# Kernel optimization log

Measured on AMD Instinct MI355X. Metric: run time of the kernel, lower is better.

The kernel has to match this reference:

```python
import jax, jax.numpy as jnp
import numpy as np

D, DFF, H, NLAYERS, B, L, U = 1536, 2048, 8, 2, 16, 64, 64
EPS = 1e-5


def _ln(x, w, b):
    mu = jnp.mean(x, axis=-1, keepdims=True)
    var = jnp.mean((x - mu) ** 2, axis=-1, keepdims=True)
    return (x - mu) / jnp.sqrt(var + EPS) * w + b


def _mha(q_in, kv_in, qkv_w, qkv_b, out_w, out_b, mask):
    # torch nn.MultiheadAttention: packed in_proj [3D,D], out_proj [D,D]
    d = q_in.shape[-1]
    hd = d // H
    wq, wk, wv = jnp.split(qkv_w, 3, axis=0)
    bq, bk, bv = jnp.split(qkv_b, 3, axis=0)
    q = q_in @ wq.T + bq
    k = kv_in @ wk.T + bk
    v = kv_in @ wv.T + bv
    def heads(t):
        b_, s_, _ = t.shape
        return t.reshape(b_, s_, H, hd).transpose(0, 2, 1, 3)  # [B,H,S,hd]
    q, k, v = heads(q), heads(k), heads(v)
    scores = jnp.einsum('bhqd,bhkd->bhqk', q, k) / jnp.sqrt(jnp.float32(hd))
    if mask is not None:
        scores = scores + mask  # [Sq,Sk] broadcast
    attn = jax.nn.softmax(scores, axis=-1)
    o = jnp.einsum('bhqk,bhkd->bhqd', attn, v)
    b_, _, s_, _ = o.shape
    o = o.transpose(0, 2, 1, 3).reshape(b_, s_, d)
    return o @ out_w.T + out_b


def setup_inputs() -> dict:
    key = jax.random.key(0)
    ks = jax.random.split(key, 16)
    f = lambda k, shp: (jax.random.normal(k, shp, jnp.float32) * 0.02)
    Lyr = NLAYERS
    return {
        'x': jax.random.normal(ks[0], (B, L, U, D), jnp.float32),
        'pooler_w': f(ks[1], (1, D)),
        'pooler_b': jnp.zeros((1,), jnp.float32),
        'pos_embed': f(ks[2], (1, 128, D)),
        'sa_qkv_w': f(ks[3], (Lyr, 3 * D, D)),
        'sa_qkv_b': jnp.zeros((Lyr, 3 * D), jnp.float32),
        'sa_out_w': f(ks[4], (Lyr, D, D)),
        'sa_out_b': jnp.zeros((Lyr, D), jnp.float32),
        'ca_qkv_w': f(ks[5], (Lyr, 3 * D, D)),
        'ca_qkv_b': jnp.zeros((Lyr, 3 * D), jnp.float32),
        'ca_out_w': f(ks[6], (Lyr, D, D)),
        'ca_out_b': jnp.zeros((Lyr, D), jnp.float32),
        'ff1_w': f(ks[7], (Lyr, DFF, D)),
        'ff1_b': jnp.zeros((Lyr, DFF), jnp.float32),
        'ff2_w': f(ks[8], (Lyr, D, DFF)),
        'ff2_b': jnp.zeros((Lyr, D), jnp.float32),
        'ln1_w': jnp.ones((Lyr, D), jnp.float32),
        'ln1_b': jnp.zeros((Lyr, D), jnp.float32),
        'ln2_w': jnp.ones((Lyr, D), jnp.float32),
        'ln2_b': jnp.zeros((Lyr, D), jnp.float32),
        'ln3_w': jnp.ones((Lyr, D), jnp.float32),
        'ln3_b': jnp.zeros((Lyr, D), jnp.float32),
    }


def reference(x, pooler_w, pooler_b, pos_embed,
              sa_qkv_w, sa_qkv_b, sa_out_w, sa_out_b,
              ca_qkv_w, ca_qkv_b, ca_out_w, ca_out_b,
              ff1_w, ff1_b, ff2_w, ff2_b,
              ln1_w, ln1_b, ln2_w, ln2_b, ln3_w, ln3_b):
    b, l, u, d = x.shape
    # SelfAttentionPooling over utterance tokens (vectorized over dialogue dim)
    logits = jnp.einsum('blud,d->blu', x, pooler_w[0]) + pooler_b[0]
    att = jax.nn.softmax(logits, axis=-1)
    pooled = jnp.einsum('blu,blud->bld', att, x)

    pos = pos_embed[:, :l, :]
    memory = pooled + pos
    tgt = pooled + pos
    causal = jnp.triu(jnp.full((l, l), -jnp.inf, jnp.float32), 1)

    h = tgt
    for i in range(NLAYERS):
        # post-norm TransformerDecoderLayer (torch default norm_first=False)
        h = _ln(h + _mha(h, h, sa_qkv_w[i], sa_qkv_b[i], sa_out_w[i], sa_out_b[i], causal),
                ln1_w[i], ln1_b[i])
        h = _ln(h + _mha(h, memory, ca_qkv_w[i], ca_qkv_b[i], ca_out_w[i], ca_out_b[i], None),
                ln2_w[i], ln2_b[i])
        ff = jax.nn.relu(h @ ff1_w[i].T + ff1_b[i]) @ ff2_w[i].T + ff2_b[i]
        h = _ln(h + ff, ln3_w[i], ln3_b[i])

    # loop over prefixes t=1..L-1 taking the last position == causal positions 0..L-2
    return h[:, : l - 1, :]
```

## Files before the change

### kernel.cpp

```cpp
#include <hip/hip_runtime.h>
#include <math.h>

#define D_MODEL 1536
#define NH      8
#define HD      192
#define BB      16
#define LL      64
#define UU      64
#define NTOK    1024
#define EPSF    1e-5f

typedef __bf16 bf16;
typedef __bf16 bf16x4_t __attribute__((ext_vector_type(4)));
typedef __bf16 bf16x8_t __attribute__((ext_vector_type(8)));
typedef float  f32x4_t  __attribute__((ext_vector_type(4)));

__device__ __forceinline__ void gload_lds16(const bf16* g, bf16* l) {
    __builtin_amdgcn_global_load_lds((const __attribute__((address_space(1))) void*)g,
                                     (__attribute__((address_space(3))) void*)l, 16, 0, 0);
}

__global__ __launch_bounds__(256)
void cvt_all_kernel(const float* __restrict__ s0, const float* __restrict__ s1,
                    const float* __restrict__ s2, const float* __restrict__ s3,
                    const float* __restrict__ s4, const float* __restrict__ s5,
                    bf16* __restrict__ dst)
{
    const int c0 = 3538944, c1 = 4718592, c2 = 8257536,
              c3 = 9437184, c4 = 11010048, c5 = 12582912;
    for (int i = blockIdx.x * 256 + threadIdx.x; i < c5; i += gridDim.x * 256) {
        const float* s; int j;
        if      (i < c0) { s = s0; j = i; }
        else if (i < c1) { s = s1; j = i - c0; }
        else if (i < c2) { s = s2; j = i - c1; }
        else if (i < c3) { s = s3; j = i - c2; }
        else if (i < c4) { s = s4; j = i - c3; }
        else             { s = s5; j = i - c4; }
        const float4 v = ((const float4*)s)[j];
        bf16x4_t o = { (bf16)v.x, (bf16)v.y, (bf16)v.z, (bf16)v.w };
        ((bf16x4_t*)dst)[i] = o;
    }
}

__global__ __launch_bounds__(256)
void fusedpool_kernel(const float* __restrict__ x, const float* __restrict__ pw,
                      const float* __restrict__ pb, const float* __restrict__ pos,
                      float* __restrict__ h, bf16* __restrict__ hb,
                      bf16* __restrict__ memb)
{
    __shared__ float red[2][4];
    const int t = threadIdx.x, wave = t >> 6, lane = t & 63;
    const int bl = blockIdx.x, l = bl & (LL - 1);
    const float* xb = x + (size_t)bl * UU * D_MODEL;

    float pwr[6];
#pragma unroll
    for (int j = 0; j < 6; ++j) pwr[j] = pw[t + j * 256];
    const float pb0 = pb[0];

    float xv[2][6];
#pragma unroll
    for (int j = 0; j < 6; ++j) xv[0][j] = xb[t + j * 256];

    float m = -__builtin_inff(), den = 0.f;
    float acc[6] = {0.f, 0.f, 0.f, 0.f, 0.f, 0.f};

    for (int u = 0; u < UU; ++u) {
        const int cur = u & 1;
        if (u < UU - 1) {
            const float* xn = xb + (size_t)(u + 1) * D_MODEL;
#pragma unroll
            for (int j = 0; j < 6; ++j) xv[cur ^ 1][j] = xn[t + j * 256];
        }
        float p = 0.f;
#pragma unroll
        for (int j = 0; j < 6; ++j) p += xv[cur][j] * pwr[j];
#pragma unroll
        for (int off = 32; off; off >>= 1) p += __shfl_xor(p, off, 64);
        if (lane == 0) red[cur][wave] = p;
        __syncthreads();
        const float logit = red[cur][0] + red[cur][1] + red[cur][2] + red[cur][3] + pb0;
        const float nm = fmaxf(m, logit);
        const float sc = __expf(m - nm);
        const float w  = __expf(logit - nm);
#pragma unroll
        for (int j = 0; j < 6; ++j) acc[j] = acc[j] * sc + w * xv[cur][j];
        den = den * sc + w;
        m = nm;
    }

    const float inv = 1.f / den;
    const size_t db = (size_t)bl * D_MODEL;
    const int pp = l * D_MODEL;
#pragma unroll
    for (int j = 0; j < 6; ++j) {
        const int d = t + j * 256;
        const float v = acc[j] * inv + pos[pp + d];
        h[db + d] = v;
        hb[db + d] = (bf16)v;
        memb[db + d] = (bf16)v;
    }
}

template<int MODE, bool DUAL, bool SPLITK>
__global__ __launch_bounds__(512, 6)
void gemm8_kernel(const bf16* __restrict__ A, const bf16* __restrict__ W,
                  const float* __restrict__ bias, void* __restrict__ Cv,
                  int N, int K, int split,
                  const bf16* __restrict__ A2, const bf16* __restrict__ W2,
                  const float* __restrict__ bias2, void* __restrict__ Cv2, int N2)
{
    __shared__ bf16 As[2][64 * 64];
    __shared__ bf16 Bs[2][128 * 64];
    const int t = threadIdx.x, wave = t >> 6, lane = t & 63;

    const int T = gridDim.x, fid = blockIdx.x;
    int vid = (fid & 7) * (T >> 3) + (fid >> 3);
    const bf16* Ap = A; const bf16* Wp = W; const float* bp = bias;
    void* Cp = Cv; int Nn = N;
    if (DUAL && vid >= split) { vid -= split; Ap = A2; Wp = W2; bp = bias2; Cp = Cv2; Nn = N2; }
    int kslice = 0;
    if (SPLITK) { kslice = vid & 1; vid >>= 1; }
    const int m0 = (vid & 15) * 64;
    const int n0 = (vid >> 4) * 128;
    const int kbase = SPLITK ? kslice * (K >> 1) : 0;

    const int wm = wave >> 2, wn = wave & 3;
    const int frow = lane & 15, kq = lane >> 4, s = frow & 7;
    const int lr = lane >> 3;
    const int g8 = ((lane & 7) ^ lr) * 8;

    f32x4_t acc[2][2] = {};

    const bf16* Abase = Ap + (size_t)(m0 + wave * 8 + lr) * K + kbase + g8;
    const bf16* Wbase = Wp + (size_t)(n0 + wave * 8 + lr) * K + kbase + g8;

    auto STAGE = [&](int buf, int tile) {
        const int k0 = tile << 6;
        gload_lds16(Abase + k0, &As[buf][wave * 512]);
        gload_lds16(Wbase + k0, &Bs[buf][wave * 512]);
        gload_lds16(Wbase + k0 + (size_t)64 * K, &Bs[buf][4096 + wave * 512]);
    };
    auto COMPUTE = [&](int buf) {
#pragma unroll
        for (int kk = 0; kk < 2; ++kk) {
            const int gg = (((kk << 2) | kq) ^ s) * 8;
            bf16x8_t af[2], bv[2];
#pragma unroll
            for (int mi = 0; mi < 2; ++mi)
                af[mi] = *(const bf16x8_t*)&As[buf][(wm * 32 + mi * 16 + frow) * 64 + gg];
#pragma unroll
            for (int ni = 0; ni < 2; ++ni)
                bv[ni] = *(const bf16x8_t*)&Bs[buf][(wn * 32 + ni * 16 + frow) * 64 + gg];
#pragma unroll
            for (int mi = 0; mi < 2; ++mi)
#pragma unroll
                for (int ni = 0; ni < 2; ++ni)
                    acc[mi][ni] = __builtin_amdgcn_mfma_f32_16x16x32_bf16(af[mi], bv[ni], acc[mi][ni], 0, 0, 0);
        }
    };

    const int nt = SPLITK ? (K >> 7) : (K >> 6);
    STAGE(0, 0);
    STAGE(1, 1);
    for (int tt = 0; tt + 1 < nt; ++tt) {
        asm volatile("s_waitcnt vmcnt(3)" ::: "memory");
        __builtin_amdgcn_s_barrier();
        COMPUTE(tt & 1);
        __builtin_amdgcn_s_barrier();
        if (tt + 2 < nt) STAGE(tt & 1, tt + 2);
    }
    asm volatile("s_waitcnt vmcnt(0)" ::: "memory");
    __builtin_amdgcn_s_barrier();
    COMPUTE((nt - 1) & 1);

    float* Cpart = (float*)Cp + (SPLITK ? (size_t)kslice * NTOK * Nn : 0);
    const int crow = m0 + wm * 32 + kq * 4;
    const int ccol = n0 + wn * 32 + frow;
#pragma unroll
    for (int mi = 0; mi < 2; ++mi)
#pragma unroll
        for (int ni = 0; ni < 2; ++ni) {
            const int col = ccol + ni * 16;
            const float bvv = (SPLITK && kslice) ? 0.f : bp[col];
            const int rb = crow + mi * 16;
#pragma unroll
            for (int j = 0; j < 4; ++j) {
                float v = acc[mi][ni][j] + bvv;
                if (MODE == 0) {
                    Cpart[(size_t)(rb + j) * Nn + col] = v;
                } else {
                    ((bf16*)Cp)[(size_t)(rb + j) * Nn + col] = (bf16)fmaxf(v, 0.f);
                }
            }
        }
}

__global__ __launch_bounds__(256)
void reduce_relu_kernel(const float* __restrict__ p0, const float* __restrict__ p1,
                        bf16* __restrict__ dst, int n4)
{
    const int i = blockIdx.x * 256 + threadIdx.x;
    if (i >= n4) return;
    const float4 a = ((const float4*)p0)[i];
    const float4 b = ((const float4*)p1)[i];
    bf16x4_t o = { (bf16)fmaxf(a.x + b.x, 0.f), (bf16)fmaxf(a.y + b.y, 0.f),
                   (bf16)fmaxf(a.z + b.z, 0.f), (bf16)fmaxf(a.w + b.w, 0.f) };
    ((bf16x4_t*)dst)[i] = o;
}

template<bool CAUSAL, bool QSPLIT>
__global__ __launch_bounds__(256)
void attn_kernel(const float* __restrict__ qbuf, const float* __restrict__ qbuf2,
                 int qstride, int qoff0,
                 const float* __restrict__ kbuf, int kstride, int koff0,
                 const float* __restrict__ vbuf, int vstride, int voff0,
                 bf16* __restrict__ out)
{
    __shared__ float kv[HD * 64];
    __shared__ float sc[16 * 64];
    const int t = threadIdx.x, wave = t >> 6, lane = t & 63;
    const int bh = blockIdx.x >> 2, qh = blockIdx.x & 3;
    const int b = bh >> 3, hh = bh & 7;
    const int t0 = b * 64;
    const float scale = rsqrtf((float)HD);

    for (int i = 0; i < 48; ++i) {
        const int idx = t + i * 256;
        const int r = idx / HD, c = idx % HD;
        kv[c * 64 + (r ^ (c & 31))] = kbuf[(size_t)(t0 + r) * kstride + koff0 + hh * HD + c];
    }
    __syncthreads();

    for (int qi = 0; qi < 4; ++qi) {
        const int ql = wave * 4 + qi;
        const int q = qh * 16 + ql;
        const size_t qb0 = (size_t)(t0 + q) * qstride + qoff0 + hh * HD;
        const float* qr  = qbuf + qb0;
        const float* qr2 = QSPLIT ? (qbuf2 + qb0) : nullptr;
        float a = 0.f;
#pragma unroll 8
        for (int d = 0; d < HD; ++d) {
            const float qv = QSPLIT ? (qr[d] + qr2[d]) : qr[d];
            a += qv * kv[d * 64 + (lane ^ (d & 31))];
        }
        a *= scale;
        if (CAUSAL && lane > q) a = -__builtin_inff();
        float m = a;
#pragma unroll
        for (int off = 32; off; off >>= 1) m = fmaxf(m, __shfl_xor(m, off, 64));
        float e = (CAUSAL && lane > q) ? 0.f : __expf(a - m);
        float s = e;
#pragma unroll
        for (int off = 32; off; off >>= 1) s += __shfl_xor(s, off, 64);
        sc[ql * 64 + lane] = e / s;
    }
    __syncthreads();

    for (int i = 0; i < 48; ++i) {
        const int idx = t + i * 256;
        const int r = idx / HD, c = idx % HD;
        kv[r * HD + c] = vbuf[(size_t)(t0 + r) * vstride + voff0 + hh * HD + c];
    }
    __syncthreads();

    for (int qi = 0; qi < 4; ++qi) {
        const int ql = wave * 4 + qi;
        const int q = qh * 16 + ql;
        float o0 = 0.f, o1 = 0.f, o2 = 0.f;
#pragma unroll 8
        for (int k = 0; k < 64; ++k) {
            const float p = sc[ql * 64 + k];
            o0 += p * kv[k * HD + lane];
            o1 += p * kv[k * HD + 64 + lane];
            o2 += p * kv[k * HD + 128 + lane];
        }
        bf16* op = out + (size_t)(t0 + q) * D_MODEL + hh * HD;
        op[lane] = (bf16)o0; op[64 + lane] = (bf16)o1; op[128 + lane] = (bf16)o2;
    }
}

template<bool R2, bool SLICE>
__global__ __launch_bounds__(256)
void ln_kernel(const float* __restrict__ a, const float* __restrict__ r,
               const float* __restrict__ r2,
               const float* __restrict__ w, const float* __restrict__ bb,
               float* __restrict__ out, bf16* __restrict__ outb,
               float* __restrict__ out2)
{
    __shared__ float red[8];
    const int tok = blockIdx.x, t = threadIdx.x;
    const int wave = t >> 6, lane = t & 63;
    const float* ap = a + (size_t)tok * D_MODEL;
    const float* rp = r + (size_t)tok * D_MODEL;
    const float* rp2 = R2 ? (r2 + (size_t)tok * D_MODEL) : nullptr;
    float v[6];
    float s = 0.f;
#pragma unroll
    for (int j = 0; j < 6; ++j) {
        v[j] = ap[t + j * 256] + rp[t + j * 256];
        if (R2) v[j] += rp2[t + j * 256];
        s += v[j];
    }
#pragma unroll
    for (int off = 32; off; off >>= 1) s += __shfl_xor(s, off, 64);
    if (lane == 0) red[wave] = s;
    __syncthreads();
    const float mu = (red[0] + red[1] + red[2] + red[3]) * (1.f / D_MODEL);
    float s2 = 0.f;
#pragma unroll
    for (int j = 0; j < 6; ++j) { const float d = v[j] - mu; s2 += d * d; }
#pragma unroll
    for (int off = 32; off; off >>= 1) s2 += __shfl_xor(s2, off, 64);
    if (lane == 0) red[4 + wave] = s2;
    __syncthreads();
    const float var = (red[4] + red[5] + red[6] + red[7]) * (1.f / D_MODEL);
    const float inv = rsqrtf(var + EPSF);
    const int bq = tok >> 6, lq = tok & 63;
#pragma unroll
    for (int j = 0; j < 6; ++j) {
        const int d = t + j * 256;
        const float o = (v[j] - mu) * inv * w[d] + bb[d];
        out[(size_t)tok * D_MODEL + d] = o;
        outb[(size_t)tok * D_MODEL + d] = (bf16)o;
        if (SLICE && lq < 63) out2[(size_t)(bq * 63 + lq) * D_MODEL + d] = o;
    }
}

extern "C" void kernel_launch(void* const* d_in, const int* in_sizes, int n_in,
                              void* d_out, int out_size, void* d_ws, size_t ws_size,
                              hipStream_t stream)
{
    (void)in_sizes; (void)n_in; (void)out_size; (void)ws_size;
    const float* x        = (const float*)d_in[0];
    const float* pooler_w = (const float*)d_in[1];
    const float* pooler_b = (const float*)d_in[2];
    const float* pos      = (const float*)d_in[3];
    const float* sa_qkv_w = (const float*)d_in[4];
    const float* sa_qkv_b = (const float*)d_in[5];
    const float* sa_out_w = (const float*)d_in[6];
    const float* sa_out_b = (const float*)d_in[7];
    const float* ca_qkv_w = (const float*)d_in[8];
    const float* ca_qkv_b = (const float*)d_in[9];
    const float* ca_out_w = (const float*)d_in[10];
    const float* ca_out_b = (const float*)d_in[11];
    const float* ff1_w    = (const float*)d_in[12];
    const float* ff1_b    = (const float*)d_in[13];
    const float* ff2_w    = (const float*)d_in[14];
    const float* ff2_b    = (const float*)d_in[15];
    const float* ln1_w    = (const float*)d_in[16];
    const float* ln1_b    = (const float*)d_in[17];
    const float* ln2_w    = (const float*)d_in[18];
    const float* ln2_b    = (const float*)d_in[19];
    const float* ln3_w    = (const float*)d_in[20];
    const float* ln3_b    = (const float*)d_in[21];
    float* outp = (float*)d_out;

    char* ws = (char*)d_ws;
    size_t off = 0;
    auto alloc = [&](size_t bytes) { char* p = ws + off; off += (bytes + 255) & ~(size_t)255; return p; };

    const size_t E_QKV = (size_t)4608 * D_MODEL;
    const size_t E_SQ  = (size_t)D_MODEL * D_MODEL;
    const size_t E_F1  = (size_t)2048 * D_MODEL;

    bf16* wb_sa_qkv = (bf16*)alloc(2 * E_QKV * 2);
    bf16* wb_sa_out = (bf16*)alloc(2 * E_SQ * 2);
    bf16* wb_ca_qkv = (bf16*)alloc(2 * E_QKV * 2);
    bf16* wb_ca_out = (bf16*)alloc(2 * E_SQ * 2);
    bf16* wb_ff1    = (bf16*)alloc(2 * E_F1 * 2);
    bf16* wb_ff2    = (bf16*)alloc(2 * E_F1 * 2);
    float* h     = (float*)alloc((size_t)NTOK * D_MODEL * 4);
    bf16*  hb    = (bf16*) alloc((size_t)NTOK * D_MODEL * 2);
    bf16*  memb  = (bf16*) alloc((size_t)NTOK * D_MODEL * 2);
    float* qkv   = (float*)alloc((size_t)NTOK * 4608 * 4);
    float* cq01  = (float*)alloc((size_t)NTOK * D_MODEL * 4 * 2);
    float* ckv0  = (float*)alloc((size_t)NTOK * 3072 * 4);
    float* ckv1  = (float*)alloc((size_t)NTOK * 3072 * 4);
    bf16*  attno = (bf16*) alloc((size_t)NTOK * D_MODEL * 2);
    float* proj01= (float*)alloc((size_t)NTOK * D_MODEL * 4 * 2);
    float* f1p01 = (float*)alloc((size_t)NTOK * 2048 * 4 * 2);
    bf16*  ffmid = (bf16*) alloc((size_t)NTOK * 2048 * 2);

    float* proj1 = proj01 + (size_t)NTOK * D_MODEL;
    float* cq1   = cq01   + (size_t)NTOK * D_MODEL;
    float* f1p1  = f1p01  + (size_t)NTOK * 2048;

    cvt_all_kernel<<<2048, 256, 0, stream>>>(sa_qkv_w, sa_out_w, ca_qkv_w,
                                             ca_out_w, ff1_w, ff2_w, wb_sa_qkv);
    fusedpool_kernel<<<NTOK, 256, 0, stream>>>(x, pooler_w, pooler_b, pos, h, hb, memb);

    gemm8_kernel<0, true, false><<<768, 512, 0, stream>>>(
        memb, wb_ca_qkv + (size_t)1536 * D_MODEL, ca_qkv_b + 1536,
        ckv0, 3072, D_MODEL, 384,
        memb, wb_ca_qkv + E_QKV + (size_t)1536 * D_MODEL, ca_qkv_b + 4608 + 1536,
        ckv1, 3072);

    for (int i = 0; i < 2; ++i) {
        float* ckv = i ? ckv1 : ckv0;

        gemm8_kernel<0, false, false><<<16 * 36, 512, 0, stream>>>(
            hb, wb_sa_qkv + (size_t)i * E_QKV, sa_qkv_b + (size_t)i * 4608,
            qkv, 4608, D_MODEL, 0, nullptr, nullptr, nullptr, nullptr, 0);
        attn_kernel<true, false><<<BB * NH * 4, 256, 0, stream>>>(
            qkv, nullptr, 4608, 0, qkv, 4608, 1536, qkv, 4608, 3072, attno);
        gemm8_kernel<0, false, true><<<16 * 12 * 2, 512, 0, stream>>>(
            attno, wb_sa_out + (size_t)i * E_SQ, sa_out_b + (size_t)i * D_MODEL,
            proj01, D_MODEL, D_MODEL, 0, nullptr, nullptr, nullptr, nullptr, 0);
        ln_kernel<true, false><<<NTOK, 256, 0, stream>>>(
            h, proj01, proj1, ln1_w + i * D_MODEL, ln1_b + i * D_MODEL, h, hb, nullptr);

        gemm8_kernel<0, false, true><<<16 * 12 * 2, 512, 0, stream>>>(
            hb, wb_ca_qkv + (size_t)i * E_QKV, ca_qkv_b + (size_t)i * 4608,
            cq01, D_MODEL, D_MODEL, 0, nullptr, nullptr, nullptr, nullptr, 0);
        attn_kernel<false, true><<<BB * NH * 4, 256, 0, stream>>>(
            cq01, cq1, 1536, 0, ckv, 3072, 0, ckv, 3072, 1536, attno);
        gemm8_kernel<0, false, true><<<16 * 12 * 2, 512, 0, stream>>>(
            attno, wb_ca_out + (size_t)i * E_SQ, ca_out_b + (size_t)i * D_MODEL,
            proj01, D_MODEL, D_MODEL, 0, nullptr, nullptr, nullptr, nullptr, 0);
        ln_kernel<true, false><<<NTOK, 256, 0, stream>>>(
            h, proj01, proj1, ln2_w + i * D_MODEL, ln2_b + i * D_MODEL, h, hb, nullptr);

        gemm8_kernel<0, false, true><<<16 * 16 * 2, 512, 0, stream>>>(
            hb, wb_ff1 + (size_t)i * E_F1, ff1_b + (size_t)i * 2048,
            f1p01, 2048, D_MODEL, 0, nullptr, nullptr, nullptr, nullptr, 0);
        reduce_relu_kernel<<<2048, 256, 0, stream>>>(
            f1p01, f1p1, ffmid, NTOK * 2048 / 4);
        gemm8_kernel<0, false, true><<<16 * 12 * 2, 512, 0, stream>>>(
            ffmid, wb_ff2 + (size_t)i * E_F1, ff2_b + (size_t)i * D_MODEL,
            proj01, D_MODEL, 2048, 0, nullptr, nullptr, nullptr, nullptr, 0);
        if (i == 0)
            ln_kernel<true, false><<<NTOK, 256, 0, stream>>>(
                h, proj01, proj1, ln3_w, ln3_b, h, hb, nullptr);
        else
            ln_kernel<true, true><<<NTOK, 256, 0, stream>>>(
                h, proj01, proj1, ln3_w + D_MODEL, ln3_b + D_MODEL, h, hb, outp);
    }
}
```

Before: 682.2 us.

## Split-K by 4 for square GEMMs, bf16 QKV/KV buffers, merge prep kernels

Several changes land together. The weight conversion and pooling kernels are merged into one launch. The self-attention QKV and cross-attention KV projections now write bf16 instead of fp32, which halves their traffic into the attention kernel. The out-projection, cross-Q and FF2 GEMMs move from split-K 2 to split-K 4, giving 768 blocks instead of 384 for better CU fill. The cost is that LayerNorm and the attention Q load must now sum four fp32 partials, and storing Q/K/V in bf16 adds some precision loss.

```diff
diff --git a/kernel.cpp b/kernel.cpp
--- a/kernel.cpp
+++ b/kernel.cpp
@@ -21,35 +21,35 @@
 }
 
 __global__ __launch_bounds__(256)
-void cvt_all_kernel(const float* __restrict__ s0, const float* __restrict__ s1,
-                    const float* __restrict__ s2, const float* __restrict__ s3,
-                    const float* __restrict__ s4, const float* __restrict__ s5,
-                    bf16* __restrict__ dst)
-{
-    const int c0 = 3538944, c1 = 4718592, c2 = 8257536,
-              c3 = 9437184, c4 = 11010048, c5 = 12582912;
-    for (int i = blockIdx.x * 256 + threadIdx.x; i < c5; i += gridDim.x * 256) {
-        const float* s; int j;
-        if      (i < c0) { s = s0; j = i; }
-        else if (i < c1) { s = s1; j = i - c0; }
-        else if (i < c2) { s = s2; j = i - c1; }
-        else if (i < c3) { s = s3; j = i - c2; }
-        else if (i < c4) { s = s4; j = i - c3; }
-        else             { s = s5; j = i - c4; }
-        const float4 v = ((const float4*)s)[j];
-        bf16x4_t o = { (bf16)v.x, (bf16)v.y, (bf16)v.z, (bf16)v.w };
-        ((bf16x4_t*)dst)[i] = o;
-    }
-}
-
-__global__ __launch_bounds__(256)
-void fusedpool_kernel(const float* __restrict__ x, const float* __restrict__ pw,
-                      const float* __restrict__ pb, const float* __restrict__ pos,
-                      float* __restrict__ h, bf16* __restrict__ hb,
-                      bf16* __restrict__ memb)
-{
+void prep_kernel(const float* __restrict__ x, const float* __restrict__ pw,
+                 const float* __restrict__ pb, const float* __restrict__ pos,
+                 float* __restrict__ h, bf16* __restrict__ hb,
+                 bf16* __restrict__ memb,
+                 const float* __restrict__ s0, const float* __restrict__ s1,
+                 const float* __restrict__ s2, const float* __restrict__ s3,
+                 const float* __restrict__ s4, const float* __restrict__ s5,
+                 bf16* __restrict__ dst)
+{
+    const int t = threadIdx.x;
+    if (blockIdx.x >= 1024) {
+        const int c0 = 3538944, c1 = 4718592, c2 = 8257536,
+                  c3 = 9437184, c4 = 11010048, c5 = 12582912;
+        for (int i = (blockIdx.x - 1024) * 256 + t; i < c5; i += 2048 * 256) {
+            const float* s; int j;
+            if      (i < c0) { s = s0; j = i; }
+            else if (i < c1) { s = s1; j = i - c0; }
+            else if (i < c2) { s = s2; j = i - c1; }
+            else if (i < c3) { s = s3; j = i - c2; }
+            else if (i < c4) { s = s4; j = i - c3; }
+            else             { s = s5; j = i - c4; }
+            const float4 v = ((const float4*)s)[j];
+            bf16x4_t o = { (bf16)v.x, (bf16)v.y, (bf16)v.z, (bf16)v.w };
+            ((bf16x4_t*)dst)[i] = o;
+        }
+        return;
+    }
     __shared__ float red[2][4];
-    const int t = threadIdx.x, wave = t >> 6, lane = t & 63;
+    const int wave = t >> 6, lane = t & 63;
     const int bl = blockIdx.x, l = bl & (LL - 1);
     const float* xb = x + (size_t)bl * UU * D_MODEL;
 
@@ -102,7 +102,7 @@
     }
 }
 
-template<int MODE, bool DUAL, bool SPLITK>
+template<int MODE, bool DUAL, int SPLITK>
 __global__ __launch_bounds__(512, 6)
 void gemm8_kernel(const bf16* __restrict__ A, const bf16* __restrict__ W,
                   const float* __restrict__ bias, void* __restrict__ Cv,
@@ -120,10 +120,12 @@
     void* Cp = Cv; int Nn = N;
     if (DUAL && vid >= split) { vid -= split; Ap = A2; Wp = W2; bp = bias2; Cp = Cv2; Nn = N2; }
     int kslice = 0;
-    if (SPLITK) { kslice = vid & 1; vid >>= 1; }
+    if (SPLITK == 2) { kslice = vid & 1; vid >>= 1; }
+    else if (SPLITK == 4) { kslice = vid & 3; vid >>= 2; }
     const int m0 = (vid & 15) * 64;
     const int n0 = (vid >> 4) * 128;
-    const int kbase = SPLITK ? kslice * (K >> 1) : 0;
+    const int Kl = SPLITK ? K / SPLITK : K;
+    const int kbase = kslice * Kl;
 
     const int wm = wave >> 2, wn = wave & 3;
     const int frow = lane & 15, kq = lane >> 4, s = frow & 7;
@@ -160,7 +162,7 @@
         }
     };
 
-    const int nt = SPLITK ? (K >> 7) : (K >> 6);
+    const int nt = Kl >> 6;
     STAGE(0, 0);
     STAGE(1, 1);
     for (int tt = 0; tt + 1 < nt; ++tt) {
@@ -189,8 +191,10 @@
                 float v = acc[mi][ni][j] + bvv;
                 if (MODE == 0) {
                     Cpart[(size_t)(rb + j) * Nn + col] = v;
+                } else if (MODE == 1) {
+                    ((bf16*)Cp)[(size_t)(rb + j) * Nn + col] = (bf16)fmaxf(v, 0.f);
                 } else {
-                    ((bf16*)Cp)[(size_t)(rb + j) * Nn + col] = (bf16)fmaxf(v, 0.f);
+                    ((bf16*)Cp)[(size_t)(rb + j) * Nn + col] = (bf16)v;
                 }
             }
         }
@@ -209,12 +213,12 @@
     ((bf16x4_t*)dst)[i] = o;
 }
 
-template<bool CAUSAL, bool QSPLIT>
+template<bool CAUSAL, bool Q4>
 __global__ __launch_bounds__(256)
-void attn_kernel(const float* __restrict__ qbuf, const float* __restrict__ qbuf2,
+void attn_kernel(const bf16* __restrict__ qb, const float* __restrict__ qp, int PN,
                  int qstride, int qoff0,
-                 const float* __restrict__ kbuf, int kstride, int koff0,
-                 const float* __restrict__ vbuf, int vstride, int voff0,
+                 const bf16* __restrict__ kbuf, int kstride, int koff0,
+                 const bf16* __restrict__ vbuf, int vstride, int voff0,
                  bf16* __restrict__ out)
 {
     __shared__ float kv[HD * 64];
@@ -228,7 +232,8 @@
     for (int i = 0; i < 48; ++i) {
         const int idx = t + i * 256;
         const int r = idx / HD, c = idx % HD;
-        kv[c * 64 + (r ^ (c & 31))] = kbuf[(size_t)(t0 + r) * kstride + koff0 + hh * HD + c];
+        kv[c * 64 + (r ^ (c & 31))] =
+            (float)kbuf[(size_t)(t0 + r) * kstride + koff0 + hh * HD + c];
     }
     __syncthreads();
 
@@ -236,12 +241,13 @@
         const int ql = wave * 4 + qi;
         const int q = qh * 16 + ql;
         const size_t qb0 = (size_t)(t0 + q) * qstride + qoff0 + hh * HD;
-        const float* qr  = qbuf + qb0;
-        const float* qr2 = QSPLIT ? (qbuf2 + qb0) : nullptr;
         float a = 0.f;
 #pragma unroll 8
         for (int d = 0; d < HD; ++d) {
-            const float qv = QSPLIT ? (qr[d] + qr2[d]) : qr[d];
+            float qv;
+            if (Q4) qv = qp[qb0 + d] + qp[(size_t)PN + qb0 + d]
+                       + qp[2 * (size_t)PN + qb0 + d] + qp[3 * (size_t)PN + qb0 + d];
+            else    qv = (float)qb[qb0 + d];
             a += qv * kv[d * 64 + (lane ^ (d & 31))];
         }
         a *= scale;
@@ -260,7 +266,7 @@
     for (int i = 0; i < 48; ++i) {
         const int idx = t + i * 256;
         const int r = idx / HD, c = idx % HD;
-        kv[r * HD + c] = vbuf[(size_t)(t0 + r) * vstride + voff0 + hh * HD + c];
+        kv[r * HD + c] = (float)vbuf[(size_t)(t0 + r) * vstride + voff0 + hh * HD + c];
     }
     __syncthreads();
 
@@ -280,10 +286,9 @@
     }
 }
 
-template<bool R2, bool SLICE>
+template<bool SLICE>
 __global__ __launch_bounds__(256)
-void ln_kernel(const float* __restrict__ a, const float* __restrict__ r,
-               const float* __restrict__ r2,
+void ln_kernel(const float* __restrict__ a, const float* __restrict__ p, int PN,
                const float* __restrict__ w, const float* __restrict__ bb,
                float* __restrict__ out, bf16* __restrict__ outb,
                float* __restrict__ out2)
@@ -292,14 +297,14 @@
     const int tok = blockIdx.x, t = threadIdx.x;
     const int wave = t >> 6, lane = t & 63;
     const float* ap = a + (size_t)tok * D_MODEL;
-    const float* rp = r + (size_t)tok * D_MODEL;
-    const float* rp2 = R2 ? (r2 + (size_t)tok * D_MODEL) : nullptr;
+    const float* pp = p + (size_t)tok * D_MODEL;
     float v[6];
     float s = 0.f;
 #pragma unroll
     for (int j = 0; j < 6; ++j) {
-        v[j] = ap[t + j * 256] + rp[t + j * 256];
-        if (R2) v[j] += rp2[t + j * 256];
+        const int d = t + j * 256;
+        v[j] = ap[d] + pp[d] + pp[(size_t)PN + d]
+             + pp[2 * (size_t)PN + d] + pp[3 * (size_t)PN + d];
         s += v[j];
     }
 #pragma unroll
@@ -363,6 +368,7 @@
     const size_t E_QKV = (size_t)4608 * D_MODEL;
     const size_t E_SQ  = (size_t)D_MODEL * D_MODEL;
     const size_t E_F1  = (size_t)2048 * D_MODEL;
+    const int    PN    = NTOK * D_MODEL;
 
     bf16* wb_sa_qkv = (bf16*)alloc(2 * E_QKV * 2);
     bf16* wb_sa_out = (bf16*)alloc(2 * E_SQ * 2);
@@ -373,67 +379,65 @@
     float* h     = (float*)alloc((size_t)NTOK * D_MODEL * 4);
     bf16*  hb    = (bf16*) alloc((size_t)NTOK * D_MODEL * 2);
     bf16*  memb  = (bf16*) alloc((size_t)NTOK * D_MODEL * 2);
-    float* qkv   = (float*)alloc((size_t)NTOK * 4608 * 4);
-    float* cq01  = (float*)alloc((size_t)NTOK * D_MODEL * 4 * 2);
-    float* ckv0  = (float*)alloc((size_t)NTOK * 3072 * 4);
-    float* ckv1  = (float*)alloc((size_t)NTOK * 3072 * 4);
+    bf16*  qkvb  = (bf16*) alloc((size_t)NTOK * 4608 * 2);
+    float* cq4   = (float*)alloc((size_t)PN * 4 * 4);
+    bf16*  ckv0  = (bf16*) alloc((size_t)NTOK * 3072 * 2);
+    bf16*  ckv1  = (bf16*) alloc((size_t)NTOK * 3072 * 2);
     bf16*  attno = (bf16*) alloc((size_t)NTOK * D_MODEL * 2);
-    float* proj01= (float*)alloc((size_t)NTOK * D_MODEL * 4 * 2);
+    float* proj4 = (float*)alloc((size_t)PN * 4 * 4);
     float* f1p01 = (float*)alloc((size_t)NTOK * 2048 * 4 * 2);
     bf16*  ffmid = (bf16*) alloc((size_t)NTOK * 2048 * 2);
 
-    float* proj1 = proj01 + (size_t)NTOK * D_MODEL;
-    float* cq1   = cq01   + (size_t)NTOK * D_MODEL;
-    float* f1p1  = f1p01  + (size_t)NTOK * 2048;
-
-    cvt_all_kernel<<<2048, 256, 0, stream>>>(sa_qkv_w, sa_out_w, ca_qkv_w,
-                                             ca_out_w, ff1_w, ff2_w, wb_sa_qkv);
-    fusedpool_kernel<<<NTOK, 256, 0, stream>>>(x, pooler_w, pooler_b, pos, h, hb, memb);
-
-    gemm8_kernel<0, true, false><<<768, 512, 0, stream>>>(
+    float* f1p1 = f1p01 + (size_t)NTOK * 2048;
+
+    prep_kernel<<<3072, 256, 0, stream>>>(x, pooler_w, pooler_b, pos, h, hb, memb,
+                                          sa_qkv_w, sa_out_w, ca_qkv_w,
+                                          ca_out_w, ff1_w, ff2_w, wb_sa_qkv);
+
+    gemm8_kernel<2, true, 0><<<768, 512, 0, stream>>>(
         memb, wb_ca_qkv + (size_t)1536 * D_MODEL, ca_qkv_b + 1536,
         ckv0, 3072, D_MODEL, 384,
         memb, wb_ca_qkv + E_QKV + (size_t)1536 * D_MODEL, ca_qkv_b + 4608 + 1536,
         ckv1, 3072);
 
     for (int i = 0; i < 2; ++i) {
-        float* ckv = i ? ckv1 : ckv0;
-
-        gemm8_kernel<0, false, false><<<16 * 36, 512, 0, stream>>>(
+        bf16* ckv = i ? ckv1 : ckv0;
+
+        gemm8_kernel<2, false, 0><<<16 * 36, 512, 0, stream>>>(
             hb, wb_sa_qkv + (size_t)i * E_QKV, sa_qkv_b + (size_t)i * 4608,
-            qkv, 4608, D_MODEL, 0, nullptr, nullptr, nullptr, nullptr, 0);
+            qkvb, 4608, D_MODEL, 0, nullptr, nullptr, nullptr, nullptr, 0);
         attn_kernel<true, false><<<BB * NH * 4, 256, 0, stream>>>(
-            qkv, nullptr, 4608, 0, qkv, 4608, 1536, qkv, 4608, 3072, attno);
-        gemm8_kernel<0, false, true><<<16 * 12 * 2, 512, 0, stream>>>(
+            qkvb, nullptr, 0, 4608, 0, qkvb, 4608, 1536, qkvb, 4608, 3072, attno);
+        gemm8_kernel<0, false, 4><<<16 * 12 * 4, 512, 0, stream>>>(
             attno, wb_sa_out + (size_t)i * E_SQ, sa_out_b + (size_t)i * D_MODEL,
-            proj01, D_MODEL, D_MODEL, 0, nullptr, nullptr, nullptr, nullptr, 0);
-        ln_kernel<true, false><<<NTOK, 256, 0, stream>>>(
-            h, proj01, proj1, ln1_w + i * D_MODEL, ln1_b + i * D_MODEL, h, hb, nullptr);
-
-        gemm8_kernel<0, false, true><<<16 * 12 * 2, 512, 0, stream>>>(
+            proj4, D_MODEL, D_MODEL, 0, nullptr, nullptr, nullptr, nullptr, 0);
+        ln_kernel<false><<<NTOK, 256, 0, stream>>>(
+            h, proj4, PN, ln1_w + i * D_MODEL, ln1_b + i * D_MODEL, h, hb, nullptr);
+
+        gemm8_kernel<0, false, 4><<<16 * 12 * 4, 512, 0, stream>>>(
             hb, wb_ca_qkv + (size_t)i * E_QKV, ca_qkv_b + (size_t)i * 4608,
-            cq01, D_MODEL, D_MODEL, 0, nullptr, nullptr, nullptr, nullptr, 0);
+            cq4, D_MODEL, D_MODEL, 0, nullptr, nullptr, nullptr, nullptr, 0);
         attn_kernel<false, true><<<BB * NH * 4, 256, 0, stream>>>(
-            cq01, cq1, 1536, 0, ckv, 3072, 0, ckv, 3072, 1536, attno);
-        gemm8_kernel<0, false, true><<<16 * 12 * 2, 512, 0, stream>>>(
+            nullptr, cq4, PN, 1536, 0, ckv, 3072, 0, ckv, 3072, 1536, attno);
+        gemm8_kernel<0, false, 4><<<16 * 12 * 4, 512, 0, stream>>>(
             attno, wb_ca_out + (size_t)i * E_SQ, ca_out_b + (size_t)i * D_MODEL,
-            proj01, D_MODEL, D_MODEL, 0, nullptr, nullptr, nullptr, nullptr, 0);
-        ln_kernel<true, false><<<NTOK, 256, 0, stream>>>(
-            h, proj01, proj1, ln2_w + i * D_MODEL, ln2_b + i * D_MODEL, h, hb, nullptr);
-
-        gemm8_kernel<0, false, true><<<16 * 16 * 2, 512, 0, stream>>>(
+            proj4, D_MODEL, D_MODEL, 0, nullptr, nullptr, nullptr, nullptr, 0);
+        ln_kernel<false><<<NTOK, 256, 0, stream>>>(
+            h, proj4, PN, ln2_w + i * D_MODEL, ln2_b + i * D_MODEL, h, hb, nullptr);
+
+        gemm8_kernel<0, false, 2><<<16 * 16 * 2, 512, 0, stream>>>(
             hb, wb_ff1 + (size_t)i * E_F1, ff1_b + (size_t)i * 2048,
             f1p01, 2048, D_MODEL, 0, nullptr, nullptr, nullptr, nullptr, 0);
         reduce_relu_kernel<<<2048, 256, 0, stream>>>(
             f1p01, f1p1, ffmid, NTOK * 2048 / 4);
-        gemm8_kernel<0, false, true><<<16 * 12 * 2, 512, 0, stream>>>(
+        gemm8_kernel<0, false, 4><<<16 * 12 * 4, 512, 0, stream>>>(
             ffmid, wb_ff2 + (size_t)i * E_F1, ff2_b + (size_t)i * D_MODEL,
-            proj01, D_MODEL, 2048, 0, nullptr, nullptr, nullptr, nullptr, 0);
+            proj4, D_MODEL, 2048, 0, nullptr, nullptr, nullptr, nullptr, 0);
         if (i == 0)
-            ln_kernel<true, false><<<NTOK, 256, 0, stream>>>(
-                h, proj01, proj1, ln3_w, ln3_b, h, hb, nullptr);
+            ln_kernel<false><<<NTOK, 256, 0, stream>>>(
+                h, proj4, PN, ln3_w, ln3_b, h, hb, nullptr);
         else
-            ln_kernel<true, true><<<NTOK, 256, 0, stream>>>(
-                h, proj01, proj1, ln3_w + D_MODEL, ln3_b + D_MODEL, h, hb, outp);
-    }
-}
+            ln_kernel<true><<<NTOK, 256, 0, stream>>>(
+                h, proj4, PN, ln3_w + D_MODEL, ln3_b + D_MODEL, h, hb, outp);
+    }
+}
```

Measured after the change: 686.2 us. About the same (+0.6%).
